# Kernel tuning notes

Measured on AMD Instinct MI355X. Metric: run time of the kernel, lower is better.

Reference implementation:

```python
import jax, jax.numpy as jnp
import numpy as np

B, T, N, D, S, V, H = 8, 256, 32, 128, 8, 32000, 4
CHUNK = 8

def _ln(x, g, b, eps=1e-5):
    m = x.mean(-1, keepdims=True)
    v = ((x - m) ** 2).mean(-1, keepdims=True)
    return (x - m) / jnp.sqrt(v + eps) * g + b

def _gelu(x):
    return jax.nn.gelu(x, approximate=False)

def setup_inputs() -> dict:
    key = jax.random.key(0)
    ks = iter(jax.random.split(key, 64))
    def nrm(shape, scale=0.02):
        return jax.random.normal(next(ks), shape, jnp.float32) * scale
    def brain(din):
        w = jax.random.normal(next(ks), (N, din, D), jnp.float32) / np.sqrt(din)
        return w, jnp.zeros((N, D), jnp.float32)
    inp = {}
    inp['idx'] = jax.random.randint(next(ks), (B, T), 0, V)
    inp['emb'] = nrm((V, D))
    inp['pos_emb'] = nrm((T, D))
    inp['ifc_w'] = nrm((D, D)); inp['ifc_b'] = jnp.zeros((D,))
    inp['ifc_g'] = jnp.ones((D,)); inp['ifc_beta'] = jnp.zeros((D,))
    inp['sproj_w'] = nrm((D, S * D)); inp['sproj_b'] = jnp.zeros((S * D,))
    inp['sgate_w'] = nrm((2 * D, D)); inp['sgate_b'] = jnp.zeros((D,))
    for name, din in [('P', 3 * D), ('D1', 2 * D), ('D2', D), ('A', D), ('G', 2 * D), ('SM', D), ('PR', D)]:
        w, b = brain(din)
        inp[name + '_w'] = w; inp[name + '_b'] = b
    for name in ['cq', 'ck', 'cv', 'co']:
        inp[name + '_w'] = nrm((D, D)); inp[name + '_b'] = jnp.zeros((D,))
    inp['cln_g'] = jnp.ones((D,)); inp['cln_b'] = jnp.zeros((D,))
    inp['sal_w'] = nrm((D, 1)); inp['sal_b'] = jnp.zeros((1,))
    inp['bcast_w'] = nrm((D, D)); inp['bcast_b'] = jnp.zeros((D,))
    inp['wln_g'] = jnp.ones((D,)); inp['wln_b'] = jnp.zeros((D,))
    inp['res_w'] = nrm((D, D)); inp['res_b'] = jnp.zeros((D,))
    inp['out_w'] = nrm((2 * D, D)); inp['out_b'] = jnp.zeros((D,))
    inp['out_bias'] = jnp.zeros((V,))
    inp['ln_g'] = jnp.ones((D,)); inp['ln_b'] = jnp.zeros((D,))
    return inp

def reference(idx, emb, pos_emb, ifc_w, ifc_b, ifc_g, ifc_beta, sproj_w, sproj_b,
              sgate_w, sgate_b, P_w, P_b, D1_w, D1_b, D2_w, D2_b, A_w, A_b, G_w, G_b,
              SM_w, SM_b, PR_w, PR_b, cq_w, cq_b, ck_w, ck_b, cv_w, cv_b, co_w, co_b,
              cln_g, cln_b, sal_w, sal_b, bcast_w, bcast_b, wln_g, wln_b,
              res_w, res_b, out_w, out_b, out_bias, ln_g, ln_b):
    # Embed + interface (eval mode: dropout = identity, no gumbel / training noise)
    raw = emb[idx] + pos_emb[:T][None]  # (B,T,D)
    percepts = _ln(_gelu(raw @ ifc_w + ifc_b), ifc_g, ifc_beta)
    pc = percepts.reshape(B, T // CHUNK, CHUNK, D).transpose(1, 2, 0, 3)  # (nC,CHUNK,B,D)

    def brain_apply(x, w, b):  # per-agent bmm: (B,N,din) x (N,din,D)
        return jnp.einsum('bni,nio->bno', x, w) + b

    def timestep(carry, cur):  # cur: (B,D)
        states, _ = carry
        sensory = (cur @ sproj_w + sproj_b).reshape(B, S, D)
        cs = states[:, :S]
        sg = jax.nn.sigmoid(jnp.concatenate([cs, sensory], -1) @ sgate_w + sgate_b)
        states = jnp.concatenate([sg * cs + (1 - sg) * sensory, states[:, S:]], axis=1)
        sal = (states @ sal_w).squeeze(-1) + sal_b[0]  # (B,N)
        wts = jax.nn.softmax(sal * 5.0, -1)
        workspace = jnp.einsum('bnd,bn->bd', states, wts)
        bcast = _ln(workspace @ bcast_w + bcast_b, wln_g, wln_b)  # (B,D), same for all N
        residual = cur @ res_w + res_b
        proj = _gelu(jnp.concatenate([workspace, residual], -1) @ out_w + out_b)
        logits = proj @ emb.T + out_bias
        return (states, bcast), logits

    def chunk_step(carry, chunk):
        states, prev_pred, has_pred, boredom = carry
        (states, bcast), logits = jax.lax.scan(timestep, (states, jnp.zeros((B, D))), chunk)
        # swarm multi-head cross-attention between agents
        hd = D // H
        def heads(x):
            return x.reshape(B, N, H, hd).transpose(0, 2, 1, 3)
        Q = heads(states @ cq_w + cq_b)
        K = heads(states @ ck_w + ck_b)
        Vv = heads(states @ cv_w + cv_b)
        attn = jax.nn.softmax(Q @ K.transpose(0, 1, 3, 2) / jnp.sqrt(jnp.float32(hd)), -1)
        msg = (attn @ Vv).transpose(0, 2, 1, 3).reshape(B, N, D)
        states = _ln(states + msg @ co_w + co_b, cln_g, cln_b)
        incoming = jnp.broadcast_to(states.mean(1, keepdims=True), (B, N, D))
        # agent_step (eval): surprise gating + EMA boredom + gated recurrent update
        pred_err = ((incoming - prev_pred) ** 2).mean(-1)  # (B,N)
        surprise = jnp.where(has_pred > 0, jax.nn.sigmoid(pred_err * 10.0), 0.0)
        incoming = incoming * (1 + surprise[..., None] * 0.5)
        boredom = 0.99 * boredom + 0.01 * (1 - jax.lax.stop_gradient(surprise).mean(0))
        broadcast = jnp.broadcast_to(bcast[:, None, :], (B, N, D))
        p_in = jnp.concatenate([incoming, broadcast, states], -1)
        perception = _gelu(brain_apply(p_in, P_w, P_b))
        self_pred = brain_apply(states, SM_w, SM_b)
        d_in = jnp.concatenate([perception, self_pred], -1)
        decision = brain_apply(_gelu(brain_apply(d_in, D1_w, D1_b)), D2_w, D2_b)
        g = jax.nn.sigmoid(brain_apply(jnp.concatenate([states, decision], -1), G_w, G_b))
        new_states = _ln(g * decision + (1 - g) * states, ln_g, ln_b)
        prediction = brain_apply(new_states, PR_w, PR_b)
        return (new_states, prediction, jnp.float32(1.0), boredom), logits

    init = (jnp.zeros((B, N, D)), jnp.zeros((B, N, D)), jnp.float32(0.0), jnp.zeros((N,)))
    _, logits = jax.lax.scan(chunk_step, init, pc)  # (nC,CHUNK,B,V)
    return logits.transpose(2, 0, 1, 3).reshape(B, T, V)
```

## Files before the change

### kernel.cpp

```cpp
#include <hip/hip_runtime.h>
#include <hip/hip_bf16.h>

#define B_ 8
#define T_ 256
#define N_ 32
#define D_ 128
#define S_ 8
#define V_ 32000
#define H_ 4
#define HD_ 32
#define NCHUNK 32
#define CH_ 8

__device__ __forceinline__ float gelu_f(float x){
    return 0.5f * x * (1.0f + erff(x * 0.70710678118654752440f));
}
__device__ __forceinline__ float sigm(float x){
    return 1.0f / (1.0f + expf(-x));
}

typedef __attribute__((ext_vector_type(4))) float f32x4v;

__global__ void k_percepts(const int* __restrict__ idx, const float* __restrict__ emb,
                           const float* __restrict__ pos_emb, const float* __restrict__ ifc_w,
                           const float* __restrict__ ifc_b, const float* __restrict__ ifc_g,
                           const float* __restrict__ ifc_beta, float* __restrict__ percepts){
    int r = blockIdx.x;
    int t = r % T_;
    int d = threadIdx.x;
    __shared__ float raw[D_];
    __shared__ float red[D_];
    int tok = idx[r];
    raw[d] = emb[tok*D_ + d] + pos_emb[t*D_ + d];
    __syncthreads();
    float acc = ifc_b[d];
    #pragma unroll 8
    for (int k=0;k<D_;k++) acc += raw[k]*ifc_w[k*D_+d];
    float x = gelu_f(acc);
    red[d] = x; __syncthreads();
    for (int s=64;s>0;s>>=1){ if(d<s) red[d]+=red[d+s]; __syncthreads(); }
    float m = red[0]*(1.0f/D_); __syncthreads();
    float dv = x-m; red[d] = dv*dv; __syncthreads();
    for (int s=64;s>0;s>>=1){ if(d<s) red[d]+=red[d+s]; __syncthreads(); }
    float var = red[0]*(1.0f/D_);
    percepts[r*D_ + d] = dv * (1.0f/sqrtf(var + 1e-5f)) * ifc_g[d] + ifc_beta[d];
}

__global__ void __launch_bounds__(256) k_precomp(const float* __restrict__ percepts,
                          const float* __restrict__ sproj_w, const float* __restrict__ sproj_b,
                          const float* __restrict__ sgate_w,
                          const float* __restrict__ res_w, const float* __restrict__ res_b,
                          const float* __restrict__ out_w,
                          float* __restrict__ sensory, float* __restrict__ sg_sens,
                          float* __restrict__ outres){
    int blk = blockIdx.x;
    int b = blk >> 5, c = blk & 31;
    int tid = threadIdx.x;
    __shared__ float p[CH_][D_];
    __shared__ float sens[CH_][S_*D_];
    __shared__ float resid[CH_][D_];
    int tbase = b*T_ + c*CH_;
    for (int i = tid; i < CH_*D_; i += 256) p[i>>7][i&127] = percepts[(tbase + (i>>7))*D_ + (i&127)];
    __syncthreads();
    for (int q=0;q<4;q++){
        int sd = tid + 256*q;
        float acc[CH_];
        #pragma unroll
        for(int i=0;i<CH_;i++) acc[i] = sproj_b[sd];
        for (int k=0;k<D_;k++){
            float w = sproj_w[k*(S_*D_) + sd];
            #pragma unroll
            for(int i=0;i<CH_;i++) acc[i] += p[i][k]*w;
        }
        #pragma unroll
        for(int i=0;i<CH_;i++){
            sens[i][sd] = acc[i];
            sensory[(size_t)(tbase+i)*(S_*D_) + sd] = acc[i];
        }
    }
    __syncthreads();
    {
        int d = tid & 127, h = tid >> 7;
        float acc[4][S_];
        #pragma unroll
        for(int ii=0;ii<4;ii++)
            #pragma unroll
            for(int s=0;s<S_;s++) acc[ii][s]=0.f;
        for (int k=0;k<D_;k++){
            float w = sgate_w[(D_+k)*D_ + d];
            #pragma unroll
            for(int ii=0;ii<4;ii++){
                int i = h*4+ii;
                #pragma unroll
                for(int s=0;s<S_;s++) acc[ii][s] += sens[i][s*D_+k]*w;
            }
        }
        for(int ii=0;ii<4;ii++){ int i=h*4+ii;
            for(int s=0;s<S_;s++) sg_sens[((size_t)(tbase+i)*S_+s)*D_ + d] = acc[ii][s];
        }
    }
    __syncthreads();
    {
        int d = tid & 127, h = tid>>7;
        float acc[4];
        #pragma unroll
        for(int ii=0;ii<4;ii++) acc[ii]=res_b[d];
        for(int k=0;k<D_;k++){
            float w = res_w[k*D_+d];
            #pragma unroll
            for(int ii=0;ii<4;ii++) acc[ii] += p[h*4+ii][k]*w;
        }
        for(int ii=0;ii<4;ii++) resid[h*4+ii][d]=acc[ii];
    }
    __syncthreads();
    {
        int d = tid & 127, h = tid>>7;
        float acc[4];
        #pragma unroll
        for(int ii=0;ii<4;ii++) acc[ii]=0.f;
        for(int k=0;k<D_;k++){
            float w = out_w[(D_+k)*D_ + d];
            #pragma unroll
            for(int ii=0;ii<4;ii++) acc[ii] += resid[h*4+ii][k]*w;
        }
        for(int ii=0;ii<4;ii++) outres[(size_t)(tbase+h*4+ii)*D_ + d] = acc[ii];
    }
}

#define ST_O   0
#define SGW_O  4096
#define KT_O   20480
#define VT_O   24608
#define QT_O   28736
#define AW_O   32864
#define RED_O  33888
#define SMEM_A 33952

__global__ void __launch_bounds__(1024) k_fused(int c,
        const float* __restrict__ sensory, const float* __restrict__ sg_sens,
        const float* __restrict__ sgate_w, const float* __restrict__ sgate_b,
        const float* __restrict__ sal_w, const float* __restrict__ sal_b,
        const float* __restrict__ out_w, const float* __restrict__ out_b,
        const float* __restrict__ outres,
        const float* __restrict__ bcast_w, const float* __restrict__ bcast_b,
        const float* __restrict__ wln_g, const float* __restrict__ wln_b,
        const float* __restrict__ cq_w, const float* __restrict__ cq_b,
        const float* __restrict__ ck_w, const float* __restrict__ ck_b,
        const float* __restrict__ cv_w, const float* __restrict__ cv_b,
        const float* __restrict__ co_w, const float* __restrict__ co_b,
        const float* __restrict__ cln_g, const float* __restrict__ cln_b,
        const float* __restrict__ states, float* __restrict__ states2,
        float* __restrict__ bcastv, float* __restrict__ meanv,
        float* __restrict__ projb){
    const int b = blockIdx.x;
    const int tid = threadIdx.x;
    __shared__ float smem[SMEM_A];
    float* st  = &smem[ST_O];
    float* sgw = &smem[SGW_O];
    float* ns   = &smem[KT_O];
    float* salv = &smem[QT_O+128];
    float* wtsv = &smem[QT_O+160];
    float* wall = &smem[AW_O];
    float* red  = &smem[RED_O];

    for (int i=tid;i<N_*D_;i+=1024) st[i] = states[b*N_*D_+i];
    {
        const f32x4v* gw = reinterpret_cast<const f32x4v*>(sgate_w);
        f32x4v* lw = reinterpret_cast<f32x4v*>(sgw);
        for (int i=tid;i<D_*D_/4;i+=1024) lw[i] = gw[i];
    }
    __syncthreads();

    if (tid < 384){
        int nn = 8 + (tid>>4), l = tid&15;
        float pa = 0.f;
        #pragma unroll
        for (int j=0;j<8;j++) pa += st[nn*D_ + l + 16*j]*sal_w[l+16*j];
        #pragma unroll
        for (int off=8;off;off>>=1) pa += __shfl_down(pa, off, 16);
        if (l==0) salv[nn] = pa + sal_b[0];
    }
    __syncthreads();

    {
        const int s = tid >> 7, d = tid & 127;
        const float sgb = sgate_b[d];
        const float* stp = &st[s*D_];
        size_t gbase = ((size_t)(b*T_ + c*CH_)*S_ + s)*D_ + d;
        float sgs = sg_sens[gbase], sv = sensory[gbase];
        for (int step=0; step<CH_; step++){
            float sgs_n=0.f, sv_n=0.f;
            if (step < CH_-1){
                sgs_n = sg_sens[gbase + (size_t)(step+1)*(S_*D_)];
                sv_n  = sensory[gbase + (size_t)(step+1)*(S_*D_)];
            }
            float acc = 0.f;
            #pragma unroll 8
            for (int k=0;k<D_;k++) acc += stp[k]*sgw[k*D_+d];
            acc += sgs + sgb;
            float sg = sigm(acc);
            ns[tid] = sg*stp[d] + (1.0f-sg)*sv;
            __syncthreads();
            st[tid] = ns[tid];
            if (tid < 128){
                int nn = tid>>4, l = tid&15;
                float pa = 0.f;
                #pragma unroll
                for (int j=0;j<8;j++) pa += ns[nn*D_ + l + 16*j]*sal_w[l+16*j];
                #pragma unroll
                for (int off=8;off;off>>=1) pa += __shfl_down(pa, off, 16);
                if (l==0) salv[nn] = pa + sal_b[0];
            }
            __syncthreads();
            if (tid < 64){
                float v = (tid<N_)? salv[tid]*5.0f : -1e30f;
                float m = v;
                #pragma unroll
                for (int off=32;off;off>>=1) m = fmaxf(m, __shfl_xor(m, off, 64));
                float e = (tid<N_)? expf(v-m) : 0.f;
                float Z = e;
                #pragma unroll
                for (int off=32;off;off>>=1) Z += __shfl_xor(Z, off, 64);
                if (tid<N_) wtsv[tid] = e/Z;
            }
            __syncthreads();
            if (tid < D_){
                float w = 0.f;
                #pragma unroll 4
                for (int n=0;n<N_;n++) w += wtsv[n]*st[n*D_+tid];
                wall[step*D_+tid] = w;
            }
            __syncthreads();
            sgs = sgs_n; sv = sv_n;
        }
    }

    {
        const int stp8 = tid >> 7, dd = tid & 127;
        const int tg = b*T_ + c*CH_ + stp8;
        float a2 = out_b[dd] + outres[(size_t)tg*D_+dd];
        const float* wsp = &wall[stp8*D_];
        #pragma unroll 8
        for (int k=0;k<D_;k++) a2 += wsp[k]*out_w[k*D_+dd];
        projb[(size_t)tg*D_+dd] = gelu_f(a2);
    }
    float a3 = 0.f;
    if (tid < D_){
        a3 = bcast_b[tid];
        #pragma unroll 8
        for (int k=0;k<D_;k++) a3 += wall[7*D_+k]*bcast_w[k*D_+tid];
        float s1 = a3, s2 = a3*a3;
        #pragma unroll
        for (int off=32;off;off>>=1){ s1 += __shfl_xor(s1,off,64); s2 += __shfl_xor(s2,off,64); }
        if ((tid&63)==0){ red[(tid>>6)*2]=s1; red[(tid>>6)*2+1]=s2; }
    }
    __syncthreads();
    if (tid < D_){
        float s1 = red[0]+red[2], s2 = red[1]+red[3];
        float mb = s1*(1.0f/D_);
        float vb = s2*(1.0f/D_) - mb*mb;
        bcastv[b*D_+tid] = (a3-mb)*(1.0f/sqrtf(vb+1e-5f))*wln_g[tid]+wln_b[tid];
    }

    {
        const int g = tid >> 7, d2 = tid & 127;
        float aK[4], aV[4], aQ[4];
        #pragma unroll
        for (int q=0;q<4;q++){ aK[q]=ck_b[d2]; aV[q]=cv_b[d2]; aQ[q]=cq_b[d2]; }
        #pragma unroll 4
        for (int k=0;k<D_;k++){
            float wq = cq_w[k*D_+d2];
            float wk = ck_w[k*D_+d2];
            float wv = cv_w[k*D_+d2];
            #pragma unroll
            for (int q=0;q<4;q++){
                float x = st[(q*8+g)*D_+k];
                aQ[q] += x*wq; aK[q] += x*wk; aV[q] += x*wv;
            }
        }
        #pragma unroll
        for (int q=0;q<4;q++){
            smem[KT_O+(q*8+g)*129+d2] = aK[q];
            smem[VT_O+(q*8+g)*129+d2] = aV[q];
            smem[QT_O+(q*8+g)*129+d2] = aQ[q];
        }
        __syncthreads();
        for (int ni=0;ni<4;ni++){
            const int n = ni*8+g;
            {
                const int h = d2>>5, m = d2&31;
                float sdot = 0.f;
                #pragma unroll
                for (int j=0;j<HD_;j++) sdot += smem[QT_O+n*129+h*32+j]*smem[KT_O+m*129+h*32+j];
                sdot *= 0.17677669529663687f;
                float mx = sdot;
                #pragma unroll
                for (int off=16;off;off>>=1) mx = fmaxf(mx, __shfl_xor(mx, off, 32));
                float e = expf(sdot-mx);
                float Z = e;
                #pragma unroll
                for (int off=16;off;off>>=1) Z += __shfl_xor(Z, off, 32);
                smem[AW_O+g*128+h*32+m] = e/Z;
            }
            __syncthreads();
            {
                const int h2 = d2>>5;
                float mm = 0.f;
                #pragma unroll 8
                for (int m2=0;m2<N_;m2++) mm += smem[AW_O+g*128+h2*32+m2]*smem[VT_O+m2*129+d2];
                smem[QT_O+n*129+d2] = mm;
            }
            __syncthreads();
        }
        float acc2[4];
        #pragma unroll
        for (int q=0;q<4;q++) acc2[q] = co_b[d2];
        #pragma unroll 4
        for (int k=0;k<D_;k++){
            float w = co_w[k*D_+d2];
            #pragma unroll
            for (int q=0;q<4;q++) acc2[q] += smem[QT_O+(q*8+g)*129+k]*w;
        }
        for (int q=0;q<4;q++){
            const int n = q*8+g;
            float x = st[n*D_+d2] + acc2[q];
            float s1 = x, s2 = x*x;
            #pragma unroll
            for (int off=32;off;off>>=1){
                s1 += __shfl_xor(s1, off, 64);
                s2 += __shfl_xor(s2, off, 64);
            }
            if ((d2&63)==0){
                smem[RED_O + g*4 + (d2>>6)*2    ] = s1;
                smem[RED_O + g*4 + (d2>>6)*2 + 1] = s2;
            }
            __syncthreads();
            s1 = smem[RED_O+g*4]   + smem[RED_O+g*4+2];
            s2 = smem[RED_O+g*4+1] + smem[RED_O+g*4+3];
            float mn  = s1*(1.0f/D_);
            float var = s2*(1.0f/D_) - mn*mn;
            float st2v = (x-mn)*(1.0f/sqrtf(var+1e-5f))*cln_g[d2]+cln_b[d2];
            states2[((size_t)b*N_+n)*D_+d2] = st2v;
            st[n*D_+d2] = st2v;
            __syncthreads();
        }
        if (tid < D_){
            float sm_ = 0.f;
            #pragma unroll 4
            for (int n2=0;n2<N_;n2++) sm_ += st[n2*D_+tid];
            meanv[b*D_+tid] = sm_*(1.0f/N_);
        }
    }
}

__global__ void __launch_bounds__(1024) k_brains(int c,
        const float* __restrict__ states2, const float* __restrict__ bcast,
        const float* __restrict__ meanv,
        const float* __restrict__ P_w, const float* __restrict__ P_b,
        const float* __restrict__ D1_w, const float* __restrict__ D1_b,
        const float* __restrict__ D2_w, const float* __restrict__ D2_b,
        const float* __restrict__ G_w, const float* __restrict__ G_b,
        const float* __restrict__ SM_w, const float* __restrict__ SM_b,
        const float* __restrict__ PR_w, const float* __restrict__ PR_b,
        const float* __restrict__ ln_g, const float* __restrict__ ln_b,
        float* __restrict__ states, float* __restrict__ prediction){
    int blk = blockIdx.x;
    int x8 = blk & 7, qq = blk >> 3;
    int n = x8 + 8*(qq & 3), b = qq >> 2;
    int tid = threadIdx.x, d = tid & 127, h = tid >> 7;
    __shared__ float strow[D_], incv[D_], bcv[D_];
    __shared__ float din[2*D_];
    __shared__ float h1v[D_], dec[D_], nsv[D_];
    __shared__ float part[1024];
    __shared__ float red[8];
    const size_t rowb = ((size_t)b*N_+n)*D_;
    if (h==0){
        float sv = states2[rowb+d]; strow[d]=sv;
        float iv = meanv[b*D_+d];   incv[d]=iv;
        float pr = prediction[rowb+d];
        float df = iv - pr;
        float s1 = df*df;
        #pragma unroll
        for (int off=32;off;off>>=1) s1 += __shfl_xor(s1, off, 64);
        if ((tid&63)==0) red[tid>>6] = s1;
    } else if (h==1){
        bcv[d] = bcast[b*D_+d];
    }
    __syncthreads();
    float pe = (red[0]+red[1])*(1.0f/D_);
    float scale = (c>0)? (1.0f + 0.5f*sigm(pe*10.0f)) : 1.0f;
    {
        float a = 0.f;
        if (h < 6){
            int src = h >> 1;
            const float* xv = (src==0)? incv : (src==1)? bcv : strow;
            int k0 = (h&1)*64;
            const float* Wn = P_w + ((size_t)n*384 + src*128 + k0)*D_ + d;
            #pragma unroll 4
            for (int k=0;k<64;k++) a += xv[k0+k]*Wn[(size_t)k*D_];
        } else {
            int k0 = (h&1)*64;
            const float* Wn = SM_w + ((size_t)n*128 + k0)*D_ + d;
            #pragma unroll 4
            for (int k=0;k<64;k++) a += strow[k0+k]*Wn[(size_t)k*D_];
        }
        part[tid] = a;
    }
    __syncthreads();
    if (h==0){
        float v = scale*(part[d]+part[128+d]) + part[256+d]+part[384+d]+part[512+d]+part[640+d] + P_b[n*D_+d];
        din[d] = gelu_f(v);
    } else if (h==1){
        din[D_+d] = part[768+d]+part[896+d] + SM_b[n*D_+d];
    }
    __syncthreads();
    {
        const float* Wn = D1_w + ((size_t)n*256 + h*32)*D_ + d;
        float a=0;
        #pragma unroll 4
        for (int k=0;k<32;k++) a += din[h*32+k]*Wn[(size_t)k*D_];
        part[tid]=a;
    }
    __syncthreads();
    if (h==0){
        float v = part[d]+part[128+d]+part[256+d]+part[384+d]+part[512+d]+part[640+d]+part[768+d]+part[896+d] + D1_b[n*D_+d];
        h1v[d] = gelu_f(v);
    }
    __syncthreads();
    {
        const float* Wn = D2_w + ((size_t)n*128 + h*16)*D_ + d;
        float a=0;
        #pragma unroll
        for (int k=0;k<16;k++) a += h1v[h*16+k]*Wn[(size_t)k*D_];
        part[tid]=a;
    }
    __syncthreads();
    if (h==0){
        dec[d] = part[d]+part[128+d]+part[256+d]+part[384+d]+part[512+d]+part[640+d]+part[768+d]+part[896+d] + D2_b[n*D_+d];
    }
    __syncthreads();
    {
        float a=0;
        if (h < 4){
            const float* Wn = G_w + ((size_t)n*256 + h*32)*D_ + d;
            #pragma unroll 4
            for (int k=0;k<32;k++) a += strow[h*32+k]*Wn[(size_t)k*D_];
        } else {
            const float* Wn = G_w + ((size_t)n*256 + 128 + (h-4)*32)*D_ + d;
            #pragma unroll 4
            for (int k=0;k<32;k++) a += dec[(h-4)*32+k]*Wn[(size_t)k*D_];
        }
        part[tid]=a;
    }
    __syncthreads();
    if (h==0){
        float gg = sigm(part[d]+part[128+d]+part[256+d]+part[384+d]+part[512+d]+part[640+d]+part[768+d]+part[896+d] + G_b[n*D_+d]);
        float pre = gg*dec[d] + (1.0f-gg)*strow[d];
        nsv[d] = pre;
        float s1 = pre, s2 = pre*pre;
        #pragma unroll
        for (int off=32;off;off>>=1){ s1 += __shfl_xor(s1, off, 64); s2 += __shfl_xor(s2, off, 64); }
        if ((tid&63)==0){ red[(tid>>6)*2]=s1; red[(tid>>6)*2+1]=s2; }
    }
    __syncthreads();
    if (h==0){
        float s1 = red[0]+red[2], s2 = red[1]+red[3];
        float mn = s1*(1.0f/D_);
        float var = s2*(1.0f/D_) - mn*mn;
        float pre = nsv[d];
        float nv = (pre-mn)*(1.0f/sqrtf(var+1e-5f))*ln_g[d]+ln_b[d];
        nsv[d]=nv;
        states[rowb+d]=nv;
    }
    __syncthreads();
    {
        const float* Wn = PR_w + ((size_t)n*128 + h*16)*D_ + d;
        float a=0;
        #pragma unroll
        for (int k=0;k<16;k++) a += nsv[h*16+k]*Wn[(size_t)k*D_];
        part[tid]=a;
    }
    __syncthreads();
    if (h==0){
        prediction[rowb+d] = part[d]+part[128+d]+part[256+d]+part[384+d]+part[512+d]+part[640+d]+part[768+d]+part[896+d] + PR_b[n*D_+d];
    }
}

__global__ void k_tobf16(const float* __restrict__ src, __hip_bfloat16* __restrict__ dst, int nelem){
    int i = blockIdx.x*256 + threadIdx.x;
    int stride = gridDim.x*256;
    for (; i<nelem; i+=stride) dst[i] = __float2bfloat16(src[i]);
}

typedef __attribute__((ext_vector_type(8))) short short8;
typedef __attribute__((ext_vector_type(4))) float f32x4;

__global__ void __launch_bounds__(256) k_gemm(const __hip_bfloat16* __restrict__ A,
                       const __hip_bfloat16* __restrict__ Bv,
                       const float* __restrict__ out_bias,
                       float* __restrict__ out){
    int vblk = blockIdx.x;
    int mblk = blockIdx.y;
    int tid = threadIdx.x;
    int wave = tid >> 6, lane = tid & 63;
    int l16 = lane & 15, quad = lane >> 4;
    int mrow = mblk*64 + wave*16 + l16;
    f32x4 acc[16];
    #pragma unroll
    for (int j=0;j<16;j++){ f32x4 z = {0.f,0.f,0.f,0.f}; acc[j]=z; }
    short8 afr[4];
    const short* Ap = reinterpret_cast<const short*>(A);
    #pragma unroll
    for (int ks=0;ks<4;ks++)
        afr[ks] = *reinterpret_cast<const short8*>(Ap + mrow*128 + ks*32 + quad*8);
    const short* Bp = reinterpret_cast<const short*>(Bv);
    int vcolbase = vblk*256;
    #pragma unroll
    for (int jj=0;jj<16;jj++){
        int v = vcolbase + jj*16 + l16;
        #pragma unroll
        for (int ks=0;ks<4;ks++){
            short8 bfr = *reinterpret_cast<const short8*>(Bp + (size_t)v*128 + ks*32 + quad*8);
            acc[jj] = __builtin_amdgcn_mfma_f32_16x16x32_bf16(afr[ks], bfr, acc[jj], 0,0,0);
        }
    }
    int mbase = mblk*64 + wave*16 + quad*4;
    #pragma unroll
    for (int jj=0;jj<16;jj++){
        int v = vcolbase + jj*16 + l16;
        float bias = out_bias[v];
        #pragma unroll
        for (int r=0;r<4;r++){
            out[(size_t)(mbase+r)*V_ + v] = acc[jj][r] + bias;
        }
    }
}

extern "C" void kernel_launch(void* const* d_in, const int* in_sizes, int n_in,
                              void* d_out, int out_size, void* d_ws, size_t ws_size,
                              hipStream_t stream){
    (void)in_sizes; (void)n_in; (void)out_size; (void)ws_size;
    const int*   idx      = (const int*)  d_in[0];
    const float* emb      = (const float*)d_in[1];
    const float* pos_emb  = (const float*)d_in[2];
    const float* ifc_w    = (const float*)d_in[3];
    const float* ifc_b    = (const float*)d_in[4];
    const float* ifc_g    = (const float*)d_in[5];
    const float* ifc_beta = (const float*)d_in[6];
    const float* sproj_w  = (const float*)d_in[7];
    const float* sproj_b  = (const float*)d_in[8];
    const float* sgate_w  = (const float*)d_in[9];
    const float* sgate_b  = (const float*)d_in[10];
    const float* P_w  = (const float*)d_in[11];
    const float* P_b  = (const float*)d_in[12];
    const float* D1_w = (const float*)d_in[13];
    const float* D1_b = (const float*)d_in[14];
    const float* D2_w = (const float*)d_in[15];
    const float* D2_b = (const float*)d_in[16];
    const float* G_w  = (const float*)d_in[19];
    const float* G_b  = (const float*)d_in[20];
    const float* SM_w = (const float*)d_in[21];
    const float* SM_b = (const float*)d_in[22];
    const float* PR_w = (const float*)d_in[23];
    const float* PR_b = (const float*)d_in[24];
    const float* cq_w = (const float*)d_in[25];
    const float* cq_b = (const float*)d_in[26];
    const float* ck_w = (const float*)d_in[27];
    const float* ck_b = (const float*)d_in[28];
    const float* cv_w = (const float*)d_in[29];
    const float* cv_b = (const float*)d_in[30];
    const float* co_w = (const float*)d_in[31];
    const float* co_b = (const float*)d_in[32];
    const float* cln_g = (const float*)d_in[33];
    const float* cln_b = (const float*)d_in[34];
    const float* sal_w = (const float*)d_in[35];
    const float* sal_b = (const float*)d_in[36];
    const float* bcast_w = (const float*)d_in[37];
    const float* bcast_b = (const float*)d_in[38];
    const float* wln_g = (const float*)d_in[39];
    const float* wln_b = (const float*)d_in[40];
    const float* res_w = (const float*)d_in[41];
    const float* res_b = (const float*)d_in[42];
    const float* out_w = (const float*)d_in[43];
    const float* out_b = (const float*)d_in[44];
    const float* out_bias = (const float*)d_in[45];
    const float* ln_g = (const float*)d_in[46];
    const float* ln_b = (const float*)d_in[47];

    float* ws = (float*)d_ws;
    float* states     = ws + 0;
    float* prediction = ws + 32768;
    float* states2    = ws + 65536;
    float* bcastv     = ws + 98304;
    float* meanv      = ws + 99328;
    float* percepts   = ws + 197632;
    float* sensory    = ws + 459776;
    float* sg_sens    = ws + 2556928;
    float* outresb    = ws + 4654080;
    float* projb      = ws + 4916224;
    __hip_bfloat16* proj_bf = (__hip_bfloat16*)(ws + 5178368);
    __hip_bfloat16* emb_bf  = (__hip_bfloat16*)(ws + 5309440);

    hipMemsetAsync(states, 0, 2*32768*sizeof(float), stream);

    k_tobf16<<<512,256,0,stream>>>(emb, emb_bf, V_*D_);
    k_percepts<<<B_*T_,128,0,stream>>>(idx, emb, pos_emb, ifc_w, ifc_b, ifc_g, ifc_beta, percepts);
    k_precomp<<<256,256,0,stream>>>(percepts, sproj_w, sproj_b, sgate_w, res_w, res_b, out_w,
                                    sensory, sg_sens, outresb);
    for (int c=0;c<NCHUNK;c++){
        k_fused<<<B_,1024,0,stream>>>(c, sensory, sg_sens, sgate_w, sgate_b, sal_w, sal_b,
                                      out_w, out_b, outresb, bcast_w, bcast_b, wln_g, wln_b,
                                      cq_w,cq_b, ck_w,ck_b, cv_w,cv_b, co_w,co_b, cln_g,cln_b,
                                      states, states2, bcastv, meanv, projb);
        k_brains<<<256,1024,0,stream>>>(c, states2, bcastv, meanv, P_w,P_b,D1_w,D1_b,D2_w,D2_b,
                                        G_w,G_b,SM_w,SM_b,PR_w,PR_b, ln_g,ln_b,
                                        states, prediction);
    }
    k_tobf16<<<256,256,0,stream>>>(projb, proj_bf, B_*T_*D_);
    k_gemm<<<dim3(125,32),256,0,stream>>>(proj_bf, emb_bf, out_bias, (float*)d_out);
}
```

Measured before the change: 3.653 ms.

## Move cross-agent attention and LayerNorm from 8-block scan into 256-block brains kernel

Measured after the change: 3.643 ms. No clear change (-0.3%).

```diff
diff --git a/kernel.cpp b/kernel.cpp
--- a/kernel.cpp
+++ b/kernel.cpp
@@ -129,14 +129,14 @@
 
 #define ST_O   0
 #define SGW_O  4096
-#define KT_O   20480
-#define VT_O   24608
-#define QT_O   28736
-#define AW_O   32864
-#define RED_O  33888
-#define SMEM_A 33952
-
-__global__ void __launch_bounds__(1024) k_fused(int c,
+#define NS_O   20480
+#define WALL_O 21504
+#define SALV_O 22528
+#define WTSV_O 22560
+#define RED_O  22592
+#define SMEM_S 22656
+
+__global__ void __launch_bounds__(1024) k_scan(int c,
         const float* __restrict__ sensory, const float* __restrict__ sg_sens,
         const float* __restrict__ sgate_w, const float* __restrict__ sgate_b,
         const float* __restrict__ sal_w, const float* __restrict__ sal_b,
@@ -147,23 +147,22 @@
         const float* __restrict__ cq_w, const float* __restrict__ cq_b,
         const float* __restrict__ ck_w, const float* __restrict__ ck_b,
         const float* __restrict__ cv_w, const float* __restrict__ cv_b,
-        const float* __restrict__ co_w, const float* __restrict__ co_b,
-        const float* __restrict__ cln_g, const float* __restrict__ cln_b,
-        const float* __restrict__ states, float* __restrict__ states2,
-        float* __restrict__ bcastv, float* __restrict__ meanv,
+        const float* __restrict__ st_in, float* __restrict__ scanA,
+        float* __restrict__ bcastv,
+        float* __restrict__ Qg, float* __restrict__ Kg, float* __restrict__ Vg,
         float* __restrict__ projb){
     const int b = blockIdx.x;
     const int tid = threadIdx.x;
-    __shared__ float smem[SMEM_A];
-    float* st  = &smem[ST_O];
-    float* sgw = &smem[SGW_O];
-    float* ns   = &smem[KT_O];
-    float* salv = &smem[QT_O+128];
-    float* wtsv = &smem[QT_O+160];
-    float* wall = &smem[AW_O];
+    __shared__ float smem[SMEM_S];
+    float* st   = &smem[ST_O];
+    float* sgw  = &smem[SGW_O];
+    float* ns   = &smem[NS_O];
+    float* wall = &smem[WALL_O];
+    float* salv = &smem[SALV_O];
+    float* wtsv = &smem[WTSV_O];
     float* red  = &smem[RED_O];
 
-    for (int i=tid;i<N_*D_;i+=1024) st[i] = states[b*N_*D_+i];
+    for (int i=tid;i<N_*D_;i+=1024) st[i] = st_in[(size_t)b*N_*D_+i];
     {
         const f32x4v* gw = reinterpret_cast<const f32x4v*>(sgate_w);
         f32x4v* lw = reinterpret_cast<f32x4v*>(sgw);
@@ -261,7 +260,7 @@
         float vb = s2*(1.0f/D_) - mb*mb;
         bcastv[b*D_+tid] = (a3-mb)*(1.0f/sqrtf(vb+1e-5f))*wln_g[tid]+wln_b[tid];
     }
-
+    scanA[b*S_*D_ + tid] = st[tid];
     {
         const int g = tid >> 7, d2 = tid & 127;
         float aK[4], aV[4], aQ[4];
@@ -280,82 +279,34 @@
         }
         #pragma unroll
         for (int q=0;q<4;q++){
-            smem[KT_O+(q*8+g)*129+d2] = aK[q];
-            smem[VT_O+(q*8+g)*129+d2] = aV[q];
-            smem[QT_O+(q*8+g)*129+d2] = aQ[q];
-        }
-        __syncthreads();
-        for (int ni=0;ni<4;ni++){
-            const int n = ni*8+g;
-            {
-                const int h = d2>>5, m = d2&31;
-                float sdot = 0.f;
-                #pragma unroll
-                for (int j=0;j<HD_;j++) sdot += smem[QT_O+n*129+h*32+j]*smem[KT_O+m*129+h*32+j];
-                sdot *= 0.17677669529663687f;
-                float mx = sdot;
-                #pragma unroll
-                for (int off=16;off;off>>=1) mx = fmaxf(mx, __shfl_xor(mx, off, 32));
-                float e = expf(sdot-mx);
-                float Z = e;
-                #pragma unroll
-                for (int off=16;off;off>>=1) Z += __shfl_xor(Z, off, 32);
-                smem[AW_O+g*128+h*32+m] = e/Z;
-            }
-            __syncthreads();
-            {
-                const int h2 = d2>>5;
-                float mm = 0.f;
-                #pragma unroll 8
-                for (int m2=0;m2<N_;m2++) mm += smem[AW_O+g*128+h2*32+m2]*smem[VT_O+m2*129+d2];
-                smem[QT_O+n*129+d2] = mm;
-            }
-            __syncthreads();
-        }
-        float acc2[4];
-        #pragma unroll
-        for (int q=0;q<4;q++) acc2[q] = co_b[d2];
-        #pragma unroll 4
-        for (int k=0;k<D_;k++){
-            float w = co_w[k*D_+d2];
-            #pragma unroll
-            for (int q=0;q<4;q++) acc2[q] += smem[QT_O+(q*8+g)*129+k]*w;
-        }
-        for (int q=0;q<4;q++){
-            const int n = q*8+g;
-            float x = st[n*D_+d2] + acc2[q];
-            float s1 = x, s2 = x*x;
-            #pragma unroll
-            for (int off=32;off;off>>=1){
-                s1 += __shfl_xor(s1, off, 64);
-                s2 += __shfl_xor(s2, off, 64);
-            }
-            if ((d2&63)==0){
-                smem[RED_O + g*4 + (d2>>6)*2    ] = s1;
-                smem[RED_O + g*4 + (d2>>6)*2 + 1] = s2;
-            }
-            __syncthreads();
-            s1 = smem[RED_O+g*4]   + smem[RED_O+g*4+2];
-            s2 = smem[RED_O+g*4+1] + smem[RED_O+g*4+3];
-            float mn  = s1*(1.0f/D_);
-            float var = s2*(1.0f/D_) - mn*mn;
-            float st2v = (x-mn)*(1.0f/sqrtf(var+1e-5f))*cln_g[d2]+cln_b[d2];
-            states2[((size_t)b*N_+n)*D_+d2] = st2v;
-            st[n*D_+d2] = st2v;
-            __syncthreads();
-        }
-        if (tid < D_){
-            float sm_ = 0.f;
-            #pragma unroll 4
-            for (int n2=0;n2<N_;n2++) sm_ += st[n2*D_+tid];
-            meanv[b*D_+tid] = sm_*(1.0f/N_);
-        }
-    }
-}
-
-__global__ void __launch_bounds__(1024) k_brains(int c,
-        const float* __restrict__ states2, const float* __restrict__ bcast,
-        const float* __restrict__ meanv,
+            int nb = b*N_ + q*8+g;
+            Qg[nb*D_+d2]=aQ[q]; Kg[nb*D_+d2]=aK[q]; Vg[nb*D_+d2]=aV[q];
+        }
+    }
+}
+
+#define AQT_O  0
+#define AKT_O  4128
+#define AVT_O  8256
+#define AST_O  12384
+#define AST2_O 16480
+#define AAW_O  20576
+#define ADIN_O 24672
+#define AH1_O  24928
+#define ADEC_O 25056
+#define ANSV_O 25184
+#define AINC_O 25312
+#define ABCV_O 25440
+#define APART_O 25568
+#define ARED_O 26592
+#define SMEM_B 26720
+
+__global__ void __launch_bounds__(1024) k_attnbrains(int c,
+        const float* __restrict__ st_in, const float* __restrict__ scanA,
+        const float* __restrict__ Qg, const float* __restrict__ Kg, const float* __restrict__ Vg,
+        const float* __restrict__ co_w, const float* __restrict__ co_b,
+        const float* __restrict__ cln_g, const float* __restrict__ cln_b,
+        const float* __restrict__ bcastv,
         const float* __restrict__ P_w, const float* __restrict__ P_b,
         const float* __restrict__ D1_w, const float* __restrict__ D1_b,
         const float* __restrict__ D2_w, const float* __restrict__ D2_b,
@@ -363,126 +314,205 @@
         const float* __restrict__ SM_w, const float* __restrict__ SM_b,
         const float* __restrict__ PR_w, const float* __restrict__ PR_b,
         const float* __restrict__ ln_g, const float* __restrict__ ln_b,
-        float* __restrict__ states, float* __restrict__ prediction){
+        float* __restrict__ st_out, float* __restrict__ prediction){
     int blk = blockIdx.x;
     int x8 = blk & 7, qq = blk >> 3;
     int n = x8 + 8*(qq & 3), b = qq >> 2;
-    int tid = threadIdx.x, d = tid & 127, h = tid >> 7;
-    __shared__ float strow[D_], incv[D_], bcv[D_];
-    __shared__ float din[2*D_];
-    __shared__ float h1v[D_], dec[D_], nsv[D_];
-    __shared__ float part[1024];
-    __shared__ float red[8];
+    int tid = threadIdx.x, d2 = tid & 127, g = tid >> 7;
+    __shared__ float smem[SMEM_B];
+    float* part = &smem[APART_O];
+    float* din  = &smem[ADIN_O];
+
+    for (int i=tid; i<N_*D_; i+=1024){
+        int r = i>>7, dd = i&127;
+        smem[AQT_O + r*129 + dd] = Qg[(b*N_+r)*D_+dd];
+        smem[AKT_O + r*129 + dd] = Kg[(b*N_+r)*D_+dd];
+        smem[AVT_O + r*129 + dd] = Vg[(b*N_+r)*D_+dd];
+        smem[AST_O + i] = (r<S_)? scanA[b*S_*D_ + i] : st_in[(size_t)b*N_*D_ + i];
+    }
+    if (tid < D_) smem[ABCV_O+tid] = bcastv[b*D_+tid];
+    __syncthreads();
+
+    {
+        const int h = d2>>5, m = d2&31;
+        #pragma unroll
+        for (int q=0;q<4;q++){
+            int nn = q*8+g;
+            float sdot = 0.f;
+            #pragma unroll 8
+            for (int j=0;j<HD_;j++) sdot += smem[AQT_O+nn*129+h*32+j]*smem[AKT_O+m*129+h*32+j];
+            sdot *= 0.17677669529663687f;
+            float mx = sdot;
+            #pragma unroll
+            for (int off=16;off;off>>=1) mx = fmaxf(mx, __shfl_xor(mx, off, 32));
+            float e = expf(sdot-mx);
+            float Z = e;
+            #pragma unroll
+            for (int off=16;off;off>>=1) Z += __shfl_xor(Z, off, 32);
+            smem[AAW_O+nn*128+h*32+m] = e/Z;
+        }
+    }
+    __syncthreads();
+    {
+        const int h = d2>>5;
+        #pragma unroll
+        for (int q=0;q<4;q++){
+            int nn = q*8+g;
+            float mm = 0.f;
+            #pragma unroll 8
+            for (int m2=0;m2<N_;m2++) mm += smem[AAW_O+nn*128+h*32+m2]*smem[AVT_O+m2*129+d2];
+            smem[AQT_O+nn*129+d2] = mm;
+        }
+    }
+    __syncthreads();
+    {
+        float acc2[4];
+        #pragma unroll
+        for (int q=0;q<4;q++) acc2[q] = co_b[d2];
+        #pragma unroll 4
+        for (int k=0;k<D_;k++){
+            float w = co_w[k*D_+d2];
+            #pragma unroll
+            for (int q=0;q<4;q++) acc2[q] += smem[AQT_O+(q*8+g)*129+k]*w;
+        }
+        float xv[4];
+        #pragma unroll
+        for (int q=0;q<4;q++){
+            xv[q] = smem[AST_O+(q*8+g)*D_+d2] + acc2[q];
+            float s1 = xv[q], s2 = xv[q]*xv[q];
+            #pragma unroll
+            for (int off=32;off;off>>=1){ s1 += __shfl_xor(s1,off,64); s2 += __shfl_xor(s2,off,64); }
+            if ((tid&63)==0){
+                int base = ARED_O + (g*4+q)*4 + (d2>>6)*2;
+                smem[base] = s1; smem[base+1] = s2;
+            }
+        }
+        __syncthreads();
+        #pragma unroll
+        for (int q=0;q<4;q++){
+            int base = ARED_O + (g*4+q)*4;
+            float s1 = smem[base]+smem[base+2], s2 = smem[base+1]+smem[base+3];
+            float mn  = s1*(1.0f/D_);
+            float var = s2*(1.0f/D_) - mn*mn;
+            smem[AST2_O+(q*8+g)*D_+d2] = (xv[q]-mn)*(1.0f/sqrtf(var+1e-5f))*cln_g[d2]+cln_b[d2];
+        }
+    }
+    __syncthreads();
+    if (tid < D_){
+        float sm_ = 0.f;
+        #pragma unroll 4
+        for (int n2=0;n2<N_;n2++) sm_ += smem[AST2_O+n2*D_+tid];
+        smem[AINC_O+tid] = sm_*(1.0f/N_);
+    }
+    __syncthreads();
     const size_t rowb = ((size_t)b*N_+n)*D_;
-    if (h==0){
-        float sv = states2[rowb+d]; strow[d]=sv;
-        float iv = meanv[b*D_+d];   incv[d]=iv;
-        float pr = prediction[rowb+d];
-        float df = iv - pr;
+    float* st2row = &smem[AST2_O + n*D_];
+    float* incv   = &smem[AINC_O];
+    float* bcv    = &smem[ABCV_O];
+    if (g==0){
+        float df = incv[d2] - prediction[rowb+d2];
         float s1 = df*df;
         #pragma unroll
         for (int off=32;off;off>>=1) s1 += __shfl_xor(s1, off, 64);
-        if ((tid&63)==0) red[tid>>6] = s1;
-    } else if (h==1){
-        bcv[d] = bcast[b*D_+d];
-    }
-    __syncthreads();
-    float pe = (red[0]+red[1])*(1.0f/D_);
+        if ((tid&63)==0) smem[ARED_O+(tid>>6)] = s1;
+    }
+    __syncthreads();
+    float pe = (smem[ARED_O]+smem[ARED_O+1])*(1.0f/D_);
     float scale = (c>0)? (1.0f + 0.5f*sigm(pe*10.0f)) : 1.0f;
     {
         float a = 0.f;
-        if (h < 6){
-            int src = h >> 1;
-            const float* xv = (src==0)? incv : (src==1)? bcv : strow;
-            int k0 = (h&1)*64;
-            const float* Wn = P_w + ((size_t)n*384 + src*128 + k0)*D_ + d;
+        if (g < 6){
+            int src = g >> 1;
+            const float* xv = (src==0)? incv : (src==1)? bcv : st2row;
+            int k0 = (g&1)*64;
+            const float* Wn = P_w + ((size_t)n*384 + src*128 + k0)*D_ + d2;
             #pragma unroll 4
             for (int k=0;k<64;k++) a += xv[k0+k]*Wn[(size_t)k*D_];
         } else {
-            int k0 = (h&1)*64;
-            const float* Wn = SM_w + ((size_t)n*128 + k0)*D_ + d;
+            int k0 = (g&1)*64;
+            const float* Wn = SM_w + ((size_t)n*128 + k0)*D_ + d2;
             #pragma unroll 4
-            for (int k=0;k<64;k++) a += strow[k0+k]*Wn[(size_t)k*D_];
+            for (int k=0;k<64;k++) a += st2row[k0+k]*Wn[(size_t)k*D_];
         }
         part[tid] = a;
     }
     __syncthreads();
-    if (h==0){
-        float v = scale*(part[d]+part[128+d]) + part[256+d]+part[384+d]+part[512+d]+part[640+d] + P_b[n*D_+d];
-        din[d] = gelu_f(v);
-    } else if (h==1){
-        din[D_+d] = part[768+d]+part[896+d] + SM_b[n*D_+d];
-    }
-    __syncthreads();
-    {
-        const float* Wn = D1_w + ((size_t)n*256 + h*32)*D_ + d;
+    if (g==0){
+        float v = scale*(part[d2]+part[128+d2]) + part[256+d2]+part[384+d2]+part[512+d2]+part[640+d2] + P_b[n*D_+d2];
+        din[d2] = gelu_f(v);
+    } else if (g==1){
+        din[D_+d2] = part[768+d2]+part[896+d2] + SM_b[n*D_+d2];
+    }
+    __syncthreads();
+    {
+        const float* Wn = D1_w + ((size_t)n*256 + g*32)*D_ + d2;
         float a=0;
         #pragma unroll 4
-        for (int k=0;k<32;k++) a += din[h*32+k]*Wn[(size_t)k*D_];
+        for (int k=0;k<32;k++) a += din[g*32+k]*Wn[(size_t)k*D_];
         part[tid]=a;
     }
     __syncthreads();
-    if (h==0){
-        float v = part[d]+part[128+d]+part[256+d]+part[384+d]+part[512+d]+part[640+d]+part[768+d]+part[896+d] + D1_b[n*D_+d];
-        h1v[d] = gelu_f(v);
-    }
-    __syncthreads();
-    {
-        const float* Wn = D2_w + ((size_t)n*128 + h*16)*D_ + d;
+    if (g==0){
+        float v = part[d2]+part[128+d2]+part[256+d2]+part[384+d2]+part[512+d2]+part[640+d2]+part[768+d2]+part[896+d2] + D1_b[n*D_+d2];
+        smem[AH1_O+d2] = gelu_f(v);
+    }
+    __syncthreads();
+    {
+        const float* Wn = D2_w + ((size_t)n*128 + g*16)*D_ + d2;
         float a=0;
         #pragma unroll
-        for (int k=0;k<16;k++) a += h1v[h*16+k]*Wn[(size_t)k*D_];
+        for (int k=0;k<16;k++) a += smem[AH1_O+g*16+k]*Wn[(size_t)k*D_];
         part[tid]=a;
     }
     __syncthreads();
-    if (h==0){
-        dec[d] = part[d]+part[128+d]+part[256+d]+part[384+d]+part[512+d]+part[640+d]+part[768+d]+part[896+d] + D2_b[n*D_+d];
+    if (g==0){
+        smem[ADEC_O+d2] = part[d2]+part[128+d2]+part[256+d2]+part[384+d2]+part[512+d2]+part[640+d2]+part[768+d2]+part[896+d2] + D2_b[n*D_+d2];
     }
     __syncthreads();
     {
         float a=0;
-        if (h < 4){
-            const float* Wn = G_w + ((size_t)n*256 + h*32)*D_ + d;
+        if (g < 4){
+            const float* Wn = G_w + ((size_t)n*256 + g*32)*D_ + d2;
             #pragma unroll 4
-            for (int k=0;k<32;k++) a += strow[h*32+k]*Wn[(size_t)k*D_];
+            for (int k=0;k<32;k++) a += st2row[g*32+k]*Wn[(size_t)k*D_];
         } else {
-            const float* Wn = G_w + ((size_t)n*256 + 128 + (h-4)*32)*D_ + d;
+            const float* Wn = G_w + ((size_t)n*256 + 128 + (g-4)*32)*D_ + d2;
             #pragma unroll 4
-            for (int k=0;k<32;k++) a += dec[(h-4)*32+k]*Wn[(size_t)k*D_];
+            for (int k=0;k<32;k++) a += smem[ADEC_O+(g-4)*32+k]*Wn[(size_t)k*D_];
         }
         part[tid]=a;
     }
     __syncthreads();
-    if (h==0){
-        float gg = sigm(part[d]+part[128+d]+part[256+d]+part[384+d]+part[512+d]+part[640+d]+part[768+d]+part[896+d] + G_b[n*D_+d]);
-        float pre = gg*dec[d] + (1.0f-gg)*strow[d];
-        nsv[d] = pre;
+    if (g==0){
+        float gg = sigm(part[d2]+part[128+d2]+part[256+d2]+part[384+d2]+part[512+d2]+part[640+d2]+part[768+d2]+part[896+d2] + G_b[n*D_+d2]);
+        float pre = gg*smem[ADEC_O+d2] + (1.0f-gg)*st2row[d2];
+        smem[ANSV_O+d2] = pre;
         float s1 = pre, s2 = pre*pre;
         #pragma unroll
         for (int off=32;off;off>>=1){ s1 += __shfl_xor(s1, off, 64); s2 += __shfl_xor(s2, off, 64); }
-        if ((tid&63)==0){ red[(tid>>6)*2]=s1; red[(tid>>6)*2+1]=s2; }
-    }
-    __syncthreads();
-    if (h==0){
-        float s1 = red[0]+red[2], s2 = red[1]+red[3];
+        if ((tid&63)==0){ smem[ARED_O+(tid>>6)*2]=s1; smem[ARED_O+(tid>>6)*2+1]=s2; }
+    }
+    __syncthreads();
+    if (g==0){
+        float s1 = smem[ARED_O]+smem[ARED_O+2], s2 = smem[ARED_O+1]+smem[ARED_O+3];
         float mn = s1*(1.0f/D_);
         float var = s2*(1.0f/D_) - mn*mn;
-        float pre = nsv[d];
-        float nv = (pre-mn)*(1.0f/sqrtf(var+1e-5f))*ln_g[d]+ln_b[d];
-        nsv[d]=nv;
-        states[rowb+d]=nv;
-    }
-    __syncthreads();
-    {
-        const float* Wn = PR_w + ((size_t)n*128 + h*16)*D_ + d;
+        float pre = smem[ANSV_O+d2];
+        float nv = (pre-mn)*(1.0f/sqrtf(var+1e-5f))*ln_g[d2]+ln_b[d2];
+        smem[ANSV_O+d2]=nv;
+        st_out[rowb+d2]=nv;
+    }
+    __syncthreads();
+    {
+        const float* Wn = PR_w + ((size_t)n*128 + g*16)*D_ + d2;
         float a=0;
         #pragma unroll
-        for (int k=0;k<16;k++) a += nsv[h*16+k]*Wn[(size_t)k*D_];
+        for (int k=0;k<16;k++) a += smem[ANSV_O+g*16+k]*Wn[(size_t)k*D_];
         part[tid]=a;
     }
     __syncthreads();
-    if (h==0){
-        prediction[rowb+d] = part[d]+part[128+d]+part[256+d]+part[384+d]+part[512+d]+part[640+d]+part[768+d]+part[896+d] + PR_b[n*D_+d];
+    if (g==0){
+        prediction[rowb+d2] = part[d2]+part[128+d2]+part[256+d2]+part[384+d2]+part[512+d2]+part[640+d2]+part[768+d2]+part[896+d2] + PR_b[n*D_+d2];
     }
 }
 
@@ -588,33 +618,40 @@
     const float* ln_b = (const float*)d_in[47];
 
     float* ws = (float*)d_ws;
-    float* states     = ws + 0;
+    float* stE        = ws + 0;
     float* prediction = ws + 32768;
-    float* states2    = ws + 65536;
-    float* bcastv     = ws + 98304;
-    float* meanv      = ws + 99328;
-    float* percepts   = ws + 197632;
-    float* sensory    = ws + 459776;
-    float* sg_sens    = ws + 2556928;
-    float* outresb    = ws + 4654080;
-    float* projb      = ws + 4916224;
-    __hip_bfloat16* proj_bf = (__hip_bfloat16*)(ws + 5178368);
-    __hip_bfloat16* emb_bf  = (__hip_bfloat16*)(ws + 5309440);
-
-    hipMemsetAsync(states, 0, 2*32768*sizeof(float), stream);
+    float* stO        = ws + 65536;
+    float* scanA      = ws + 98304;
+    float* bcastv     = ws + 106496;
+    float* Qg         = ws + 107520;
+    float* Kg         = ws + 140288;
+    float* Vg         = ws + 173056;
+    float* percepts   = ws + 205824;
+    float* sensory    = ws + 467968;
+    float* sg_sens    = ws + 2565120;
+    float* outresb    = ws + 4662272;
+    float* projb      = ws + 4924416;
+    __hip_bfloat16* proj_bf = (__hip_bfloat16*)(ws + 5186560);
+    __hip_bfloat16* emb_bf  = (__hip_bfloat16*)(ws + 5317632);
+
+    hipMemsetAsync(stE, 0, 2*32768*sizeof(float), stream);
 
     k_tobf16<<<512,256,0,stream>>>(emb, emb_bf, V_*D_);
     k_percepts<<<B_*T_,128,0,stream>>>(idx, emb, pos_emb, ifc_w, ifc_b, ifc_g, ifc_beta, percepts);
     k_precomp<<<256,256,0,stream>>>(percepts, sproj_w, sproj_b, sgate_w, res_w, res_b, out_w,
                                     sensory, sg_sens, outresb);
     for (int c=0;c<NCHUNK;c++){
-        k_fused<<<B_,1024,0,stream>>>(c, sensory, sg_sens, sgate_w, sgate_b, sal_w, sal_b,
-                                      out_w, out_b, outresb, bcast_w, bcast_b, wln_g, wln_b,
-                                      cq_w,cq_b, ck_w,ck_b, cv_w,cv_b, co_w,co_b, cln_g,cln_b,
-                                      states, states2, bcastv, meanv, projb);
-        k_brains<<<256,1024,0,stream>>>(c, states2, bcastv, meanv, P_w,P_b,D1_w,D1_b,D2_w,D2_b,
-                                        G_w,G_b,SM_w,SM_b,PR_w,PR_b, ln_g,ln_b,
-                                        states, prediction);
+        const float* stin = (c&1)? stO : stE;
+        float* stout      = (c&1)? stE : stO;
+        k_scan<<<B_,1024,0,stream>>>(c, sensory, sg_sens, sgate_w, sgate_b, sal_w, sal_b,
+                                     out_w, out_b, outresb, bcast_w, bcast_b, wln_g, wln_b,
+                                     cq_w,cq_b, ck_w,ck_b, cv_w,cv_b,
+                                     stin, scanA, bcastv, Qg, Kg, Vg, projb);
+        k_attnbrains<<<256,1024,0,stream>>>(c, stin, scanA, Qg, Kg, Vg, co_w, co_b,
+                                            cln_g, cln_b, bcastv,
+                                            P_w,P_b, D1_w,D1_b, D2_w,D2_b, G_w,G_b,
+                                            SM_w,SM_b, PR_w,PR_b, ln_g,ln_b,
+                                            stout, prediction);
     }
     k_tobf16<<<256,256,0,stream>>>(projb, proj_bf, B_*T_*D_);
     k_gemm<<<dim3(125,32),256,0,stream>>>(proj_bf, emb_bf, out_bias, (float*)d_out);
```
